# Performance work log

Hardware: AMD Instinct MI355X
Metric: run time of the kernel (lower is better)

Reference implementation:

```python
import jax, jax.numpy as jnp
import numpy as np

HEADS = 20
SHIFT = 0.6931471805599453  # style_alignment_score_shift = log(2)
KEY_SCALE = 1.0             # style_alignment_score_scale
EPS = 1e-5


def expand_first(feat, scale=1.0):
    # feat: [B, H, S, D]; broadcast style features (batch items 0 and B//2)
    b = feat.shape[0]
    fs = jnp.stack([feat[0], feat[b // 2]])[:, None]           # [2,1,H,S,D]
    fs = jnp.broadcast_to(fs, (2, b // 2) + feat.shape[1:])    # [2,B/2,H,S,D]
    if scale != 1:
        fs = jnp.concatenate([fs[:, :1], scale * fs[:, 1:]], axis=1)
    return fs.reshape(feat.shape)


def concat_first(feat, scale=1.0):
    # concatenate style features along the sequence axis (-2)
    return jnp.concatenate([feat, expand_first(feat, scale=scale)], axis=-2)


def adain(feat):
    # stats over sequence axis (-2); torch .var() is unbiased (ddof=1)
    mean = feat.mean(axis=-2, keepdims=True)
    std = jnp.sqrt(feat.var(axis=-2, keepdims=True, ddof=1) + EPS)
    sm = expand_first(mean)
    ss = expand_first(std)
    return (feat - mean) / std * ss + sm


def setup_inputs() -> dict:
    key = jax.random.key(0)
    ks = jax.random.split(key, 6)
    B, S, C = 4, 1024, 1280
    sc = 1.0 / np.sqrt(C)
    return {
        "hidden_states": jax.random.normal(ks[0], (B, S, C), jnp.float32),
        "Wq": jax.random.normal(ks[1], (C, C), jnp.float32) * sc,
        "Wk": jax.random.normal(ks[2], (C, C), jnp.float32) * sc,
        "Wv": jax.random.normal(ks[3], (C, C), jnp.float32) * sc,
        "Wo": jax.random.normal(ks[4], (C, C), jnp.float32) * sc,
        "bo": jnp.zeros((C,), jnp.float32),
    }


def reference(hidden_states, Wq, Wk, Wv, Wo, bo):
    B, S, C = hidden_states.shape
    H = HEADS
    hd = C // H
    scale = hd ** -0.5

    def to_heads(t):  # [B,S,C] -> [B,H,S,hd]
        return t.reshape(B, S, H, hd).transpose(0, 2, 1, 3)

    q = to_heads(hidden_states @ Wq.T)
    k = to_heads(hidden_states @ Wk.T)
    v = to_heads(hidden_states @ Wv.T)

    q = adain(q)              # adain_queries
    k = adain(k)              # adain_keys
    # adain_values = False

    k = concat_first(k, scale=KEY_SCALE)   # [B,H,2S,hd]
    v = concat_first(v)                    # [B,H,2S,hd]

    # shifted scaled dot-product attention (shift added to shared-key block)
    logits = jnp.einsum('bhqd,bhkd->bhqk', q, k) * scale  # [B,H,S,2S]
    bias = jnp.where(jnp.arange(k.shape[-2]) >= S, jnp.float32(SHIFT), jnp.float32(0.0))
    probs = jax.nn.softmax(logits + bias, axis=-1)
    out = jnp.einsum('bhqk,bhkd->bhqd', probs, v)         # [B,H,S,hd]

    out = out.transpose(0, 2, 1, 3).reshape(B, S, C)
    out = out @ Wo.T + bo
    return out
```

## Files before the change

### kernel.cpp

```cpp
#include <hip/hip_runtime.h>
#include <math.h>


typedef __bf16 bf16x8 __attribute__((ext_vector_type(8)));
typedef __bf16 bf16x2_t __attribute__((ext_vector_type(2)));
typedef float f32x4 __attribute__((ext_vector_type(4)));
typedef unsigned short u16x8 __attribute__((ext_vector_type(8)));

#define BDIM 256

__device__ inline unsigned short f2bf(float f) {
  return __builtin_bit_cast(unsigned short, (__bf16)f);
}
__device__ inline unsigned int pack_bf2(float lo, float hi) {
  bf16x2_t v;
  v[0] = (__bf16)lo;
  v[1] = (__bf16)hi;
  return __builtin_bit_cast(unsigned int, v);
}
__device__ inline float bf2f(unsigned short h) {
  return __uint_as_float(((unsigned int)h) << 16);
}

__device__ inline void gl_lds16(const unsigned short* g, unsigned short* l) {
  __builtin_amdgcn_global_load_lds(
      (const __attribute__((address_space(1))) unsigned int*)g,
      (__attribute__((address_space(3))) unsigned int*)l, 16, 0, 0);
}

__global__ __launch_bounds__(BDIM) void k_convert_all(
    const float* __restrict__ X, const float* __restrict__ Wq,
    const float* __restrict__ Wk, const float* __restrict__ Wv,
    const float* __restrict__ Wo, unsigned short* __restrict__ Xbf,
    unsigned short* __restrict__ Wcat, unsigned short* __restrict__ Wobf) {
  const int idx = blockIdx.x * BDIM + threadIdx.x;
  const float* src;
  unsigned short* dst;
  int off;
  if (idx < 1310720) {
    src = X; dst = Xbf; off = idx;
  } else {
    const int r = idx - 1310720;
    const int which = r / 409600;
    off = r - which * 409600;
    src = (which == 0) ? Wq : (which == 1) ? Wk : (which == 2) ? Wv : Wo;
    dst = (which < 3) ? Wcat + (size_t)which * 1638400 : Wobf;
  }
  const float4 v = ((const float4*)src)[off];
  ushort4 o;
  o.x = f2bf(v.x); o.y = f2bf(v.y); o.z = f2bf(v.z); o.w = f2bf(v.w);
  ((ushort4*)dst)[off] = o;
}

__global__ __launch_bounds__(512, 1) void k_gemm_bf16(
    const unsigned short* __restrict__ A, const unsigned short* __restrict__ B,
    unsigned short* __restrict__ qb, unsigned short* __restrict__ kb,
    unsigned short* __restrict__ vb, int M, int N, int K) {
  __shared__ unsigned short lds[4][2][256 * 32];

  const int bid = blockIdx.x;
  const int swz = (bid & 7) * 30 + (bid >> 3);
  const int mt = swz & 15, nt = swz >> 4;
  const int mBase = mt * 256, nBase = nt * 256;
  const int r3 = nt / 5;
  unsigned short* Cb = (r3 == 0) ? qb : (r3 == 1) ? kb : vb;
  const int nOff = nBase - r3 * 1280;

  const int t = threadIdx.x;
  const int w = t >> 6, lane = t & 63, quad = lane >> 4, l16 = lane & 15;
  const int wrow = w & 1, wcol = w >> 1;
  const int NTILES = K >> 5;

  f32x4 acc[8][4];
#pragma unroll
  for (int i = 0; i < 8; ++i)
#pragma unroll
    for (int j = 0; j < 4; ++j) acc[i][j] = (f32x4){0.f, 0.f, 0.f, 0.f};

  const int srow = t >> 2;
  const int sgl = ((t & 3) ^ ((t >> 3) & 3)) * 8;

  auto stage = [&](int s, int kt) {
#pragma unroll
    for (int j = 0; j < 2; ++j) {
      const int row = j * 128 + srow;
      gl_lds16(A + (size_t)(mBase + row) * K + kt * 32 + sgl,
               &lds[s][0][(j * 512 + t) * 8]);
    }
#pragma unroll
    for (int j = 0; j < 2; ++j) {
      const int row = j * 128 + srow;
      gl_lds16(B + (size_t)(nBase + row) * K + kt * 32 + sgl,
               &lds[s][1][(j * 512 + t) * 8]);
    }
  };

  stage(0, 0);
  stage(1, 1);

  const int arow0 = (wrow * 128 + l16) * 32;
  const int brow0 = (wcol * 64 + l16) * 32;
  const int gsw = (quad ^ ((l16 >> 1) & 3)) * 8;

  for (int kt = 0; kt < NTILES; ++kt) {
    const int s = kt & 3;
    if (kt + 2 < NTILES) {
      stage((kt + 2) & 3, kt + 2);
      asm volatile("s_waitcnt vmcnt(8)" ::: "memory");
    } else if (kt + 1 < NTILES) {
      asm volatile("s_waitcnt vmcnt(4)" ::: "memory");
    } else {
      asm volatile("s_waitcnt vmcnt(0)" ::: "memory");
    }
    __builtin_amdgcn_s_barrier();

    const unsigned short* As = &lds[s][0][0];
    const unsigned short* Bs = &lds[s][1][0];
    bf16x8 af[8], bq[4];
#pragma unroll
    for (int mi = 0; mi < 8; ++mi)
      af[mi] = *(const bf16x8*)(As + arow0 + mi * 512 + gsw);
#pragma unroll
    for (int ni = 0; ni < 4; ++ni)
      bq[ni] = *(const bf16x8*)(Bs + brow0 + ni * 512 + gsw);
    __builtin_amdgcn_s_setprio(1);
#pragma unroll
    for (int mi = 0; mi < 8; ++mi)
#pragma unroll
      for (int ni = 0; ni < 4; ++ni)
        acc[mi][ni] = __builtin_amdgcn_mfma_f32_16x16x32_bf16(
            af[mi], bq[ni], acc[mi][ni], 0, 0, 0);
    __builtin_amdgcn_s_setprio(0);
  }

#pragma unroll
  for (int mi = 0; mi < 8; ++mi)
#pragma unroll
    for (int r = 0; r < 4; ++r) {
      const int row = mBase + wrow * 128 + mi * 16 + quad * 4 + r;
#pragma unroll
      for (int ni = 0; ni < 4; ++ni)
        Cb[(size_t)row * 1280 + nOff + wcol * 64 + ni * 16 + l16] =
            f2bf(acc[mi][ni][r]);
    }
}

__global__ __launch_bounds__(BDIM, 2) void k_gemm_out(
    const unsigned short* __restrict__ A, const unsigned short* __restrict__ B,
    float* __restrict__ Cf, const float* __restrict__ bias, int M, int N,
    int K) {
  __shared__ unsigned short lds[4][2][128 * 32];

  const int bid = blockIdx.x;
  const int swz = (bid & 7) * 40 + (bid >> 3);
  const int mt = swz & 31, nt = swz >> 5;
  const int mBase = mt * 128, nBase = nt * 128;

  const int t = threadIdx.x;
  const int w = t >> 6, lane = t & 63, quad = lane >> 4, l16 = lane & 15;
  const int wrow = w & 1, wcol = w >> 1;
  const int NTILES = K >> 5;

  f32x4 acc[4][4];
#pragma unroll
  for (int i = 0; i < 4; ++i)
#pragma unroll
    for (int j = 0; j < 4; ++j) acc[i][j] = (f32x4){0.f, 0.f, 0.f, 0.f};

  const int srow = t >> 2;
  const int sgl = ((t & 3) ^ ((t >> 3) & 3)) * 8;

  auto stage = [&](int s, int kt) {
#pragma unroll
    for (int j = 0; j < 2; ++j) {
      const int row = j * 64 + srow;
      gl_lds16(A + (size_t)(mBase + row) * K + kt * 32 + sgl,
               &lds[s][0][(j * 256 + t) * 8]);
    }
#pragma unroll
    for (int j = 0; j < 2; ++j) {
      const int row = j * 64 + srow;
      gl_lds16(B + (size_t)(nBase + row) * K + kt * 32 + sgl,
               &lds[s][1][(j * 256 + t) * 8]);
    }
  };

  stage(0, 0);
  stage(1, 1);

  const int arow0 = (wrow * 64 + l16) * 32;
  const int brow0 = (wcol * 64 + l16) * 32;
  const int gsw = (quad ^ ((l16 >> 1) & 3)) * 8;

  for (int kt = 0; kt < NTILES; ++kt) {
    const int s = kt & 3;
    if (kt + 2 < NTILES) {
      stage((kt + 2) & 3, kt + 2);
      asm volatile("s_waitcnt vmcnt(8)" ::: "memory");
    } else if (kt + 1 < NTILES) {
      asm volatile("s_waitcnt vmcnt(4)" ::: "memory");
    } else {
      asm volatile("s_waitcnt vmcnt(0)" ::: "memory");
    }
    __builtin_amdgcn_s_barrier();

    const unsigned short* As = &lds[s][0][0];
    const unsigned short* Bs = &lds[s][1][0];
    bf16x8 af[4], bq[4];
#pragma unroll
    for (int mi = 0; mi < 4; ++mi)
      af[mi] = *(const bf16x8*)(As + arow0 + mi * 512 + gsw);
#pragma unroll
    for (int ni = 0; ni < 4; ++ni)
      bq[ni] = *(const bf16x8*)(Bs + brow0 + ni * 512 + gsw);
    __builtin_amdgcn_s_setprio(1);
#pragma unroll
    for (int mi = 0; mi < 4; ++mi)
#pragma unroll
      for (int ni = 0; ni < 4; ++ni)
        acc[mi][ni] = __builtin_amdgcn_mfma_f32_16x16x32_bf16(
            af[mi], bq[ni], acc[mi][ni], 0, 0, 0);
    __builtin_amdgcn_s_setprio(0);
  }

#pragma unroll
  for (int mi = 0; mi < 4; ++mi)
#pragma unroll
    for (int r = 0; r < 4; ++r) {
      const int row = mBase + wrow * 64 + mi * 16 + quad * 4 + r;
#pragma unroll
      for (int ni = 0; ni < 4; ++ni) {
        const int col = nBase + wcol * 64 + ni * 16 + l16;
        Cf[(size_t)row * N + col] = acc[mi][ni][r] + bias[col];
      }
    }
}

__global__ __launch_bounds__(320) void k_stats1(
    const unsigned short* __restrict__ qb, const unsigned short* __restrict__ kb,
    float* __restrict__ psum, float* __restrict__ psq) {
  const int z = blockIdx.y, which = z >> 2, b = z & 3;
  const unsigned short* src = (which == 0) ? qb : kb;
  const int c = threadIdx.x * 4;
  const size_t base = (size_t)(b * 1024 + blockIdx.x * 32) * 1280 + c;
  float4 s = {0.f, 0.f, 0.f, 0.f}, s2 = {0.f, 0.f, 0.f, 0.f};
#pragma unroll 8
  for (int i = 0; i < 32; ++i) {
    const ushort4 xv = *(const ushort4*)(src + base + (size_t)i * 1280);
    const float x0 = bf2f(xv.x), x1 = bf2f(xv.y), x2 = bf2f(xv.z),
                x3 = bf2f(xv.w);
    s.x += x0; s.y += x1; s.z += x2; s.w += x3;
    s2.x = fmaf(x0, x0, s2.x); s2.y = fmaf(x1, x1, s2.y);
    s2.z = fmaf(x2, x2, s2.z); s2.w = fmaf(x3, x3, s2.w);
  }
  const size_t o = ((size_t)z * 32 + blockIdx.x) * 1280 + c;
  *(float4*)(psum + o) = s;
  *(float4*)(psq + o) = s2;
}

__global__ __launch_bounds__(BDIM) void k_stats2(
    const float* __restrict__ psum, const float* __restrict__ psq,
    float* __restrict__ fst) {
  const int which = blockIdx.y;
  const int c = blockIdx.x * 256 + threadIdx.x;
  float m[4], sd[4];
#pragma unroll
  for (int b = 0; b < 4; ++b) {
    const int z = which * 4 + b;
    float s = 0.f, s2 = 0.f;
#pragma unroll
    for (int j = 0; j < 32; ++j) {
      s += psum[((size_t)z * 32 + j) * 1280 + c];
      s2 += psq[((size_t)z * 32 + j) * 1280 + c];
    }
    const float mean = s * (1.0f / 1024.0f);
    const float var = (s2 - 1024.0f * mean * mean) * (1.0f / 1023.0f);
    m[b] = mean;
    sd[b] = sqrtf(var + 1e-5f);
  }
  const float S2 = 0.125f * 1.44269504088896341f;
#pragma unroll
  for (int b = 0; b < 4; ++b) {
    const int bs = (b < 2) ? 0 : 2;
    const float g = sd[bs] / sd[b];
    const float o = m[bs] - m[b] * g;
    if (which == 0) {
      fst[(0 * 4 + b) * 1280 + c] = g;
      fst[(1 * 4 + b) * 1280 + c] = o;
    } else {
      fst[(2 * 4 + b) * 1280 + c] = g * S2;
      fst[(3 * 4 + b) * 1280 + c] = o;
    }
  }
}

__global__ __launch_bounds__(BDIM) void k_vt(
    const unsigned short* __restrict__ vb, unsigned short* __restrict__ vt) {
  __shared__ unsigned short tile[64][65];
  const int tb = blockIdx.x;
  const int b = tb / 320;
  const int r2 = tb - b * 320;
  const int c0 = (r2 / 16) * 64;
  const int s0 = (r2 & 15) * 64;
  const int t = threadIdx.x;
  const int r = t >> 2, seg = (t & 3) * 16;
  const size_t goff = ((size_t)(b * 1024 + s0 + r)) * 1280 + c0 + seg;
  const u16x8 va = *(const u16x8*)(vb + goff);
  const u16x8 vv = *(const u16x8*)(vb + goff + 8);
#pragma unroll
  for (int j = 0; j < 8; j++) {
    tile[r][seg + j] = va[j];
    tile[r][seg + 8 + j] = vv[j];
  }
  __syncthreads();
  u16x8 o0, o1;
#pragma unroll
  for (int j = 0; j < 8; j++) {
    o0[j] = tile[seg + j][r];
    o1[j] = tile[seg + 8 + j][r];
  }
  const size_t ooff = ((size_t)(b * 1280 + c0 + r)) * 1024 + s0 + seg;
  *(u16x8*)(vt + ooff) = o0;
  *(u16x8*)(vt + ooff + 8) = o1;
}

__global__ __launch_bounds__(BDIM, 4) void k_attn(
    const unsigned short* __restrict__ qb, const unsigned short* __restrict__ kb,
    const float* __restrict__ fst, const unsigned short* __restrict__ vt,
    unsigned short* __restrict__ Op0, unsigned short* __restrict__ Op1,
    float* __restrict__ Lpart) {
  const int S = 1024;
  const int L = blockIdx.x + 8 * (blockIdx.y + 20 * blockIdx.z);
  const int qt = (L >> 3) & 7;
  const int hz = (L & 7) + ((L >> 6) << 3);
  const int h = hz % 20;
  const int zs = hz / 20;
  int b, chunk;
  if (zs < 2)      { b = 0; chunk = zs; }
  else if (zs < 6) { b = 1; chunk = zs - 2; }
  else if (zs < 8) { b = 2; chunk = zs - 6; }
  else             { b = 3; chunk = zs - 8; }
  const int ktBeg = chunk * 8;
  const int t = threadIdx.x, w = t >> 6, lane = t & 63;
  const int quad = lane >> 4, l16 = lane & 15;
  const int bstyle = (b < 2) ? 0 : 2;
  const int qrow = qt * 128 + w * 32;
  const bool style = (ktBeg >= 16);

  __shared__ unsigned short Ks[2][2][64 * 32];
  __shared__ unsigned short Vs[2][64 * 32];
  __shared__ unsigned short Plds[4][32][64];

  const float S2 = 0.125f * 1.44269504088896341f;

  bf16x8 aq[2][2];
  float biasv[2];
  {
    const int bk = style ? bstyle : b;
    float rq[2] = {0.f, 0.f};
#pragma unroll
    for (int hf = 0; hf < 2; ++hf) {
      const int cc = h * 64 + quad * 8 + hf * 32;
      float gq[8], oq[8], gs[8], ok[8];
      *(float4*)(gq)     = *(const float4*)(fst + (0 * 4 + b) * 1280 + cc);
      *(float4*)(gq + 4) = *(const float4*)(fst + (0 * 4 + b) * 1280 + cc + 4);
      *(float4*)(oq)     = *(const float4*)(fst + (1 * 4 + b) * 1280 + cc);
      *(float4*)(oq + 4) = *(const float4*)(fst + (1 * 4 + b) * 1280 + cc + 4);
      *(float4*)(gs)     = *(const float4*)(fst + (2 * 4 + bk) * 1280 + cc);
      *(float4*)(gs + 4) = *(const float4*)(fst + (2 * 4 + bk) * 1280 + cc + 4);
      *(float4*)(ok)     = *(const float4*)(fst + (3 * 4 + bk) * 1280 + cc);
      *(float4*)(ok + 4) = *(const float4*)(fst + (3 * 4 + bk) * 1280 + cc + 4);
#pragma unroll
      for (int g = 0; g < 2; ++g) {
        const size_t qoff =
            ((size_t)(b * S + qrow + g * 16 + l16)) * 1280 + cc;
        const bf16x8 qv = *(const bf16x8*)(qb + qoff);
        bf16x8 av;
#pragma unroll
        for (int j = 0; j < 8; ++j) {
          const float qn = fmaf((float)qv[j], gq[j], oq[j]);
          rq[g] = fmaf(qn, ok[j], rq[g]);
          av[j] = (__bf16)(qn * gs[j]);
        }
        aq[g][hf] = av;
      }
    }
    const float shift = style ? 1.0f : 0.0f;
#pragma unroll
    for (int g = 0; g < 2; ++g) {
      float r = rq[g] * S2;
      r += __shfl_xor(r, 16, 64);
      r += __shfl_xor(r, 32, 64);
      biasv[g] = shift + r;
    }
  }

  bf16x8 ones;
#pragma unroll
  for (int i = 0; i < 8; ++i) ones[i] = (__bf16)1.0f;

  f32x4 o[2][4], lsum[2];
#pragma unroll
  for (int g = 0; g < 2; ++g) {
    lsum[g] = (f32x4){0.f, 0.f, 0.f, 0.f};
#pragma unroll
    for (int i = 0; i < 4; i++) o[g][i] = (f32x4){0.f, 0.f, 0.f, 0.f};
  }

  const int krow = t >> 2;
  const int kseg = ((t & 3) ^ ((t >> 3) & 3)) * 8;
  const int sw = l16 & 14;
  const int qsw = (quad ^ ((l16 >> 1) & 3)) * 8;

  auto stageK = [&](int buf, int kt) {
    const int bs = (kt < 16) ? b : bstyle;
    const int sk = (kt & 15) * 64;
    const unsigned short* kg =
        kb + (size_t)(bs * S + sk + krow) * 1280 + h * 64 + kseg;
    gl_lds16(kg, Ks[buf][0] + t * 8);
    gl_lds16(kg + 32, Ks[buf][1] + t * 8);
  };
  auto stageV = [&](int kt) {
    const int bs = (kt < 16) ? b : bstyle;
    const int sk = (kt & 15) * 64;
    const unsigned short* vg =
        vt + (size_t)(bs * 1280 + h * 64 + krow) * S + sk + kseg;
    gl_lds16(vg, Vs[0] + t * 8);
    gl_lds16(vg + 32, Vs[1] + t * 8);
  };

  stageK(0, ktBeg);

  for (int i = 0; i < 8; ++i) {
    const int kt = ktBeg + i;
    const int buf = i & 1;
    asm volatile("s_waitcnt vmcnt(0)" ::: "memory");
    __builtin_amdgcn_s_barrier();
    stageV(kt);
    if (i + 1 < 8) stageK(buf ^ 1, kt + 1);

    f32x4 z2[2][4];
#pragma unroll
    for (int nt = 0; nt < 4; ++nt) {
      const bf16x8 bk0 =
          *(const bf16x8*)(Ks[buf][0] + (nt * 16 + l16) * 32 + qsw);
      const bf16x8 bk1 =
          *(const bf16x8*)(Ks[buf][1] + (nt * 16 + l16) * 32 + qsw);
#pragma unroll
      for (int g = 0; g < 2; ++g) {
        f32x4 zz = (f32x4){0.f, 0.f, 0.f, 0.f};
        zz = __builtin_amdgcn_mfma_f32_16x16x32_bf16(bk0, aq[g][0], zz, 0, 0, 0);
        zz = __builtin_amdgcn_mfma_f32_16x16x32_bf16(bk1, aq[g][1], zz, 0, 0, 0);
        z2[g][nt] = zz;
      }
    }

#pragma unroll
    for (int g = 0; g < 2; ++g) {
      const float bg = biasv[g];
#pragma unroll
      for (int nt = 0; nt < 4; ++nt) {
        const float e0 = exp2f(z2[g][nt][0] + bg);
        const float e1 = exp2f(z2[g][nt][1] + bg);
        const float e2 = exp2f(z2[g][nt][2] + bg);
        const float e3 = exp2f(z2[g][nt][3] + bg);
        uint2 pk;
        pk.x = pack_bf2(e0, e1);
        pk.y = pack_bf2(e2, e3);
        const int phys = (nt * 4 + quad) ^ sw;
        *(uint2*)(&Plds[w][g * 16 + l16][phys * 4]) = pk;
      }
    }

    if (i + 1 < 8)
      asm volatile("s_waitcnt vmcnt(2)" ::: "memory");
    else
      asm volatile("s_waitcnt vmcnt(0)" ::: "memory");
    __builtin_amdgcn_s_barrier();

#pragma unroll
    for (int g = 0; g < 2; ++g) {
      const int a0 = (2 * quad) ^ sw;
      const int a1 = (2 * quad + 8) ^ sw;
      const bf16x8 pa0 = *(const bf16x8*)(&Plds[w][g * 16 + l16][a0 * 4]);
      const bf16x8 pa1 = *(const bf16x8*)(&Plds[w][g * 16 + l16][a1 * 4]);
      lsum[g] = __builtin_amdgcn_mfma_f32_16x16x32_bf16(pa0, ones, lsum[g], 0, 0, 0);
      lsum[g] = __builtin_amdgcn_mfma_f32_16x16x32_bf16(pa1, ones, lsum[g], 0, 0, 0);
#pragma unroll
      for (int dt = 0; dt < 4; ++dt) {
        const bf16x8 vb0 =
            *(const bf16x8*)(Vs[0] + (dt * 16 + l16) * 32 + qsw);
        const bf16x8 vb1 =
            *(const bf16x8*)(Vs[1] + (dt * 16 + l16) * 32 + qsw);
        o[g][dt] =
            __builtin_amdgcn_mfma_f32_16x16x32_bf16(pa0, vb0, o[g][dt], 0, 0, 0);
        o[g][dt] =
            __builtin_amdgcn_mfma_f32_16x16x32_bf16(pa1, vb1, o[g][dt], 0, 0, 0);
      }
    }
  }

  if (l16 == 0) {
#pragma unroll
    for (int g = 0; g < 2; ++g)
#pragma unroll
      for (int r = 0; r < 4; ++r)
        Lpart[((size_t)zs * 20 + h) * 1024 + qrow + g * 16 + quad * 4 + r] =
            lsum[g][r];
  }

  unsigned short* Op = (zs < 4) ? Op0 + (size_t)zs * 1310720
                                : Op1 + (size_t)(zs - 4) * 1310720;
#pragma unroll
  for (int g = 0; g < 2; ++g)
#pragma unroll
    for (int dt = 0; dt < 4; ++dt)
#pragma unroll
      for (int r = 0; r < 4; ++r)
        Op[(size_t)(qrow + g * 16 + quad * 4 + r) * 1280 + h * 64 + dt * 16 +
           l16] = f2bf(o[g][dt][r]);
}

__global__ __launch_bounds__(BDIM) void k_combine(
    const unsigned short* __restrict__ Op0, const unsigned short* __restrict__ Op1,
    const float* __restrict__ Lpart, unsigned short* __restrict__ attnb) {
  const int idx = blockIdx.x * BDIM + threadIdx.x;
  const int row = idx / 160;
  const int c = (idx - row * 160) * 8;
  const int b = row >> 10, q = row & 1023, h = c >> 6;
  const int zb = (b >> 1) * 6 + (b & 1) * 2;
  const int ns = 2 + (b & 1) * 2;
  float L = 0.f;
  float acc[8] = {0.f, 0.f, 0.f, 0.f, 0.f, 0.f, 0.f, 0.f};
  for (int s = 0; s < ns; ++s) {
    const int z = zb + s;
    const unsigned short* base = (z < 4)
        ? Op0 + (size_t)z * 1310720
        : Op1 + (size_t)(z - 4) * 1310720;
    L += Lpart[((size_t)z * 20 + h) * 1024 + q];
    const u16x8 v = *(const u16x8*)(base + (size_t)q * 1280 + c);
#pragma unroll
    for (int j = 0; j < 8; ++j) acc[j] += bf2f(v[j]);
  }
  const float rl = 1.0f / L;
  u16x8 o8;
#pragma unroll
  for (int j = 0; j < 8; ++j) o8[j] = f2bf(acc[j] * rl);
  *(u16x8*)(attnb + (size_t)row * 1280 + c) = o8;
}

extern "C" void kernel_launch(void* const* d_in, const int* in_sizes, int n_in,
                              void* d_out, int out_size, void* d_ws,
                              size_t ws_size, hipStream_t stream) {
  const float* X = (const float*)d_in[0];
  const float* Wq = (const float*)d_in[1];
  const float* Wk = (const float*)d_in[2];
  const float* Wv = (const float*)d_in[3];
  const float* Wo = (const float*)d_in[4];
  const float* bo = (const float*)d_in[5];
  float* out = (float*)d_out;

  char* ws = (char*)d_ws;
  size_t off = 0;
  auto alloc = [&](size_t bytes) {
    char* p = ws + off;
    off += (bytes + 255) & ~(size_t)255;
    return p;
  };
  unsigned short* Wcat = (unsigned short*)alloc(3840ull * 1280 * 2);
  unsigned short* Xbf = (unsigned short*)alloc(4096ull * 1280 * 2);
  unsigned short* qbb = (unsigned short*)alloc(4096ull * 1280 * 2);
  unsigned short* kbb = (unsigned short*)alloc(4096ull * 1280 * 2);
  unsigned short* vbb = (unsigned short*)alloc(4096ull * 1280 * 2);
  unsigned short* Wobf = (unsigned short*)alloc(1280ull * 1280 * 2);
  float* fstats = (float*)alloc(4ull * 4 * 1280 * 4);
  unsigned short* qnb = (unsigned short*)alloc(4096ull * 1280 * 2);
  unsigned short* knb = (unsigned short*)alloc(4096ull * 1280 * 2);
  unsigned short* vtb = (unsigned short*)alloc(4096ull * 1280 * 2);
  unsigned short* attnb = (unsigned short*)alloc(4096ull * 1280 * 2);
  (void)knb;

  unsigned short* Op0 = Xbf;
  unsigned short* Op1 = qnb;
  float* Lpart = (float*)Wcat;
  float* psum = (float*)attnb;
  float* psq = (float*)(attnb + 4096ull * 1280 / 2);

  k_convert_all<<<11520, BDIM, 0, stream>>>(X, Wq, Wk, Wv, Wo, Xbf, Wcat, Wobf);
  k_gemm_bf16<<<240, 512, 0, stream>>>(Xbf, Wcat, qbb, kbb, vbb, 4096, 3840,
                                       1280);
  k_stats1<<<dim3(32, 8), 320, 0, stream>>>(qbb, kbb, psum, psq);
  k_stats2<<<dim3(5, 2), BDIM, 0, stream>>>(psum, psq, fstats);
  k_vt<<<1280, BDIM, 0, stream>>>(vbb, vtb);
  k_attn<<<dim3(8, 20, 12), BDIM, 0, stream>>>(qbb, kbb, fstats, vtb, Op0, Op1,
                                               Lpart);
  k_combine<<<2560, BDIM, 0, stream>>>(Op0, Op1, Lpart, attnb);
  k_gemm_out<<<320, BDIM, 0, stream>>>(attnb, Wobf, out, bo, 4096, 1280, 1280);
}
```

Before: 246.4 us.

## Use longer key chunks in attention split-K and write style batches directly

Attention work is now split into 16-tile key chunks instead of 8-tile chunks. Batches 0 and 2 attend only over their own keys, so they fit in one chunk and write normalized output straight to the attention buffer. Batches 1 and 3 keep a two-way split that the combine kernel merges. The Q/AdaIN preload is moved after the first K stage is issued so the load overlaps. This halves the attention grid and the partial-sum traffic, and combine now only processes half the rows. The cost is fewer blocks (960), which may lower occupancy and parallelism across the GPU.

```diff
diff --git a/kernel.cpp b/kernel.cpp
--- a/kernel.cpp
+++ b/kernel.cpp
@@ -327,20 +327,22 @@
 __global__ __launch_bounds__(BDIM, 4) void k_attn(
     const unsigned short* __restrict__ qb, const unsigned short* __restrict__ kb,
     const float* __restrict__ fst, const unsigned short* __restrict__ vt,
-    unsigned short* __restrict__ Op0, unsigned short* __restrict__ Op1,
-    float* __restrict__ Lpart) {
+    unsigned short* __restrict__ Opart, float* __restrict__ Lpart,
+    unsigned short* __restrict__ attnb) {
   const int S = 1024;
   const int L = blockIdx.x + 8 * (blockIdx.y + 20 * blockIdx.z);
   const int qt = (L >> 3) & 7;
   const int hz = (L & 7) + ((L >> 6) << 3);
   const int h = hz % 20;
   const int zs = hz / 20;
-  int b, chunk;
-  if (zs < 2)      { b = 0; chunk = zs; }
-  else if (zs < 6) { b = 1; chunk = zs - 2; }
-  else if (zs < 8) { b = 2; chunk = zs - 6; }
-  else             { b = 3; chunk = zs - 8; }
-  const int ktBeg = chunk * 8;
+  int b, ktBeg;
+  bool direct;
+  if (zs == 0)      { b = 0; ktBeg = 0;  direct = true;  }
+  else if (zs == 1) { b = 1; ktBeg = 0;  direct = false; }
+  else if (zs == 2) { b = 1; ktBeg = 16; direct = false; }
+  else if (zs == 3) { b = 2; ktBeg = 0;  direct = true;  }
+  else if (zs == 4) { b = 3; ktBeg = 0;  direct = false; }
+  else              { b = 3; ktBeg = 16; direct = false; }
   const int t = threadIdx.x, w = t >> 6, lane = t & 63;
   const int quad = lane >> 4, l16 = lane & 15;
   const int bstyle = (b < 2) ? 0 : 2;
@@ -352,60 +354,6 @@
   __shared__ unsigned short Plds[4][32][64];
 
   const float S2 = 0.125f * 1.44269504088896341f;
-
-  bf16x8 aq[2][2];
-  float biasv[2];
-  {
-    const int bk = style ? bstyle : b;
-    float rq[2] = {0.f, 0.f};
-#pragma unroll
-    for (int hf = 0; hf < 2; ++hf) {
-      const int cc = h * 64 + quad * 8 + hf * 32;
-      float gq[8], oq[8], gs[8], ok[8];
-      *(float4*)(gq)     = *(const float4*)(fst + (0 * 4 + b) * 1280 + cc);
-      *(float4*)(gq + 4) = *(const float4*)(fst + (0 * 4 + b) * 1280 + cc + 4);
-      *(float4*)(oq)     = *(const float4*)(fst + (1 * 4 + b) * 1280 + cc);
-      *(float4*)(oq + 4) = *(const float4*)(fst + (1 * 4 + b) * 1280 + cc + 4);
-      *(float4*)(gs)     = *(const float4*)(fst + (2 * 4 + bk) * 1280 + cc);
-      *(float4*)(gs + 4) = *(const float4*)(fst + (2 * 4 + bk) * 1280 + cc + 4);
-      *(float4*)(ok)     = *(const float4*)(fst + (3 * 4 + bk) * 1280 + cc);
-      *(float4*)(ok + 4) = *(const float4*)(fst + (3 * 4 + bk) * 1280 + cc + 4);
-#pragma unroll
-      for (int g = 0; g < 2; ++g) {
-        const size_t qoff =
-            ((size_t)(b * S + qrow + g * 16 + l16)) * 1280 + cc;
-        const bf16x8 qv = *(const bf16x8*)(qb + qoff);
-        bf16x8 av;
-#pragma unroll
-        for (int j = 0; j < 8; ++j) {
-          const float qn = fmaf((float)qv[j], gq[j], oq[j]);
-          rq[g] = fmaf(qn, ok[j], rq[g]);
-          av[j] = (__bf16)(qn * gs[j]);
-        }
-        aq[g][hf] = av;
-      }
-    }
-    const float shift = style ? 1.0f : 0.0f;
-#pragma unroll
-    for (int g = 0; g < 2; ++g) {
-      float r = rq[g] * S2;
-      r += __shfl_xor(r, 16, 64);
-      r += __shfl_xor(r, 32, 64);
-      biasv[g] = shift + r;
-    }
-  }
-
-  bf16x8 ones;
-#pragma unroll
-  for (int i = 0; i < 8; ++i) ones[i] = (__bf16)1.0f;
-
-  f32x4 o[2][4], lsum[2];
-#pragma unroll
-  for (int g = 0; g < 2; ++g) {
-    lsum[g] = (f32x4){0.f, 0.f, 0.f, 0.f};
-#pragma unroll
-    for (int i = 0; i < 4; i++) o[g][i] = (f32x4){0.f, 0.f, 0.f, 0.f};
-  }
 
   const int krow = t >> 2;
   const int kseg = ((t & 3) ^ ((t >> 3) & 3)) * 8;
@@ -431,13 +379,67 @@
 
   stageK(0, ktBeg);
 
-  for (int i = 0; i < 8; ++i) {
+  bf16x8 aq[2][2];
+  float biasv[2];
+  {
+    const int bk = style ? bstyle : b;
+    float rq[2] = {0.f, 0.f};
+#pragma unroll
+    for (int hf = 0; hf < 2; ++hf) {
+      const int cc = h * 64 + quad * 8 + hf * 32;
+      float gq[8], oq[8], gs[8], ok[8];
+      *(float4*)(gq)     = *(const float4*)(fst + (0 * 4 + b) * 1280 + cc);
+      *(float4*)(gq + 4) = *(const float4*)(fst + (0 * 4 + b) * 1280 + cc + 4);
+      *(float4*)(oq)     = *(const float4*)(fst + (1 * 4 + b) * 1280 + cc);
+      *(float4*)(oq + 4) = *(const float4*)(fst + (1 * 4 + b) * 1280 + cc + 4);
+      *(float4*)(gs)     = *(const float4*)(fst + (2 * 4 + bk) * 1280 + cc);
+      *(float4*)(gs + 4) = *(const float4*)(fst + (2 * 4 + bk) * 1280 + cc + 4);
+      *(float4*)(ok)     = *(const float4*)(fst + (3 * 4 + bk) * 1280 + cc);
+      *(float4*)(ok + 4) = *(const float4*)(fst + (3 * 4 + bk) * 1280 + cc + 4);
+#pragma unroll
+      for (int g = 0; g < 2; ++g) {
+        const size_t qoff =
+            ((size_t)(b * S + qrow + g * 16 + l16)) * 1280 + cc;
+        const bf16x8 qv = *(const bf16x8*)(qb + qoff);
+        bf16x8 av;
+#pragma unroll
+        for (int j = 0; j < 8; ++j) {
+          const float qn = fmaf((float)qv[j], gq[j], oq[j]);
+          rq[g] = fmaf(qn, ok[j], rq[g]);
+          av[j] = (__bf16)(qn * gs[j]);
+        }
+        aq[g][hf] = av;
+      }
+    }
+    const float shift = style ? 1.0f : 0.0f;
+#pragma unroll
+    for (int g = 0; g < 2; ++g) {
+      float r = rq[g] * S2;
+      r += __shfl_xor(r, 16, 64);
+      r += __shfl_xor(r, 32, 64);
+      biasv[g] = shift + r;
+    }
+  }
+
+  bf16x8 ones;
+#pragma unroll
+  for (int i = 0; i < 8; ++i) ones[i] = (__bf16)1.0f;
+
+  f32x4 o[2][4], lsum[2];
+#pragma unroll
+  for (int g = 0; g < 2; ++g) {
+    lsum[g] = (f32x4){0.f, 0.f, 0.f, 0.f};
+#pragma unroll
+    for (int i = 0; i < 4; i++) o[g][i] = (f32x4){0.f, 0.f, 0.f, 0.f};
+  }
+
+  for (int i = 0; i < 16; ++i) {
     const int kt = ktBeg + i;
     const int buf = i & 1;
     asm volatile("s_waitcnt vmcnt(0)" ::: "memory");
     __builtin_amdgcn_s_barrier();
     stageV(kt);
-    if (i + 1 < 8) stageK(buf ^ 1, kt + 1);
+    if (i + 1 < 16) stageK(buf ^ 1, kt + 1);
 
     f32x4 z2[2][4];
 #pragma unroll
@@ -472,7 +474,7 @@
       }
     }
 
-    if (i + 1 < 8)
+    if (i + 1 < 16)
       asm volatile("s_waitcnt vmcnt(2)" ::: "memory");
     else
       asm volatile("s_waitcnt vmcnt(0)" ::: "memory");
@@ -500,53 +502,68 @@
     }
   }
 
-  if (l16 == 0) {
+  if (direct) {
+    unsigned short* ab =
+        attnb + ((size_t)(b * S + qrow)) * 1280 + h * 64;
 #pragma unroll
     for (int g = 0; g < 2; ++g)
 #pragma unroll
-      for (int r = 0; r < 4; ++r)
-        Lpart[((size_t)zs * 20 + h) * 1024 + qrow + g * 16 + quad * 4 + r] =
-            lsum[g][r];
-  }
-
-  unsigned short* Op = (zs < 4) ? Op0 + (size_t)zs * 1310720
-                                : Op1 + (size_t)(zs - 4) * 1310720;
-#pragma unroll
-  for (int g = 0; g < 2; ++g)
-#pragma unroll
-    for (int dt = 0; dt < 4; ++dt)
-#pragma unroll
-      for (int r = 0; r < 4; ++r)
-        Op[(size_t)(qrow + g * 16 + quad * 4 + r) * 1280 + h * 64 + dt * 16 +
-           l16] = f2bf(o[g][dt][r]);
+      for (int r = 0; r < 4; ++r) {
+        const float rl = 1.0f / lsum[g][r];
+        const int ro = (g * 16 + quad * 4 + r) * 1280;
+#pragma unroll
+        for (int dt = 0; dt < 4; ++dt)
+          ab[ro + dt * 16 + l16] = f2bf(o[g][dt][r] * rl);
+      }
+  } else {
+    const int slice = (zs < 3) ? (zs - 1) : (zs - 2);
+    if (l16 == 0) {
+#pragma unroll
+      for (int g = 0; g < 2; ++g)
+#pragma unroll
+        for (int r = 0; r < 4; ++r)
+          Lpart[((size_t)slice * 20 + h) * 1024 + qrow + g * 16 + quad * 4 +
+                r] = lsum[g][r];
+    }
+    unsigned short* Op = Opart + (size_t)slice * 1310720;
+#pragma unroll
+    for (int g = 0; g < 2; ++g)
+#pragma unroll
+      for (int dt = 0; dt < 4; ++dt)
+#pragma unroll
+        for (int r = 0; r < 4; ++r)
+          Op[(size_t)(qrow + g * 16 + quad * 4 + r) * 1280 + h * 64 + dt * 16 +
+             l16] = f2bf(o[g][dt][r]);
+  }
 }
 
 __global__ __launch_bounds__(BDIM) void k_combine(
-    const unsigned short* __restrict__ Op0, const unsigned short* __restrict__ Op1,
-    const float* __restrict__ Lpart, unsigned short* __restrict__ attnb) {
+    const unsigned short* __restrict__ Opart, const float* __restrict__ Lpart,
+    unsigned short* __restrict__ attnb) {
   const int idx = blockIdx.x * BDIM + threadIdx.x;
   const int row = idx / 160;
   const int c = (idx - row * 160) * 8;
-  const int b = row >> 10, q = row & 1023, h = c >> 6;
-  const int zb = (b >> 1) * 6 + (b & 1) * 2;
-  const int ns = 2 + (b & 1) * 2;
+  const int bb = row >> 10;
+  const int q = row & 1023;
+  const int h = c >> 6;
+  const int s0 = bb * 2;
   float L = 0.f;
   float acc[8] = {0.f, 0.f, 0.f, 0.f, 0.f, 0.f, 0.f, 0.f};
-  for (int s = 0; s < ns; ++s) {
-    const int z = zb + s;
-    const unsigned short* base = (z < 4)
-        ? Op0 + (size_t)z * 1310720
-        : Op1 + (size_t)(z - 4) * 1310720;
+#pragma unroll
+  for (int s = 0; s < 2; ++s) {
+    const int z = s0 + s;
     L += Lpart[((size_t)z * 20 + h) * 1024 + q];
-    const u16x8 v = *(const u16x8*)(base + (size_t)q * 1280 + c);
+    const u16x8 v =
+        *(const u16x8*)(Opart + (size_t)z * 1310720 + (size_t)q * 1280 + c);
 #pragma unroll
     for (int j = 0; j < 8; ++j) acc[j] += bf2f(v[j]);
   }
   const float rl = 1.0f / L;
+  const int orow = (bb * 2 + 1) * 1024 + q;
   u16x8 o8;
 #pragma unroll
   for (int j = 0; j < 8; ++j) o8[j] = f2bf(acc[j] * rl);
-  *(u16x8*)(attnb + (size_t)row * 1280 + c) = o8;
+  *(u16x8*)(attnb + (size_t)orow * 1280 + c) = o8;
 }
 
 extern "C" void kernel_launch(void* const* d_in, const int* in_sizes, int n_in,
@@ -578,10 +595,10 @@
   unsigned short* knb = (unsigned short*)alloc(4096ull * 1280 * 2);
   unsigned short* vtb = (unsigned short*)alloc(4096ull * 1280 * 2);
   unsigned short* attnb = (unsigned short*)alloc(4096ull * 1280 * 2);
+  (void)qnb;
   (void)knb;
 
-  unsigned short* Op0 = Xbf;
-  unsigned short* Op1 = qnb;
+  unsigned short* Opart = Xbf;
   float* Lpart = (float*)Wcat;
   float* psum = (float*)attnb;
   float* psq = (float*)(attnb + 4096ull * 1280 / 2);
@@ -592,8 +609,8 @@
   k_stats1<<<dim3(32, 8), 320, 0, stream>>>(qbb, kbb, psum, psq);
   k_stats2<<<dim3(5, 2), BDIM, 0, stream>>>(psum, psq, fstats);
   k_vt<<<1280, BDIM, 0, stream>>>(vbb, vtb);
-  k_attn<<<dim3(8, 20, 12), BDIM, 0, stream>>>(qbb, kbb, fstats, vtb, Op0, Op1,
-                                               Lpart);
-  k_combine<<<2560, BDIM, 0, stream>>>(Op0, Op1, Lpart, attnb);
+  k_attn<<<dim3(8, 20, 6), BDIM, 0, stream>>>(qbb, kbb, fstats, vtb, Opart,
+                                              Lpart, attnb);
+  k_combine<<<1280, BDIM, 0, stream>>>(Opart, Lpart, attnb);
   k_gemm_out<<<320, BDIM, 0, stream>>>(attnb, Wobf, out, bo, 4096, 1280, 1280);
 }
```

Result: faster. 239.3 us (-2.9%).
